# Optimization experiments

Hardware: AMD Instinct MI355X
Metric: run time of the kernel (lower is better)

The kernel has to match this reference:

```python
import jax, jax.numpy as jnp
import numpy as np
import math

B, N, H, D = 2, 2048, 16, 64

def setup_inputs() -> dict:
    key = jax.random.key(0)
    kq, kk, kv = jax.random.split(key, 3)
    q = jax.random.normal(kq, (B, N, H, D), dtype=jnp.float32)
    k = jax.random.normal(kk, (B, N, H, D), dtype=jnp.float32)
    v = jax.random.normal(kv, (B, N, H, D), dtype=jnp.float32)
    return {"q": q, "k": k, "v": v}

def reference(q, k, v):
    d = q.shape[-1]
    # [b,n,h,d] -> [b,h,n,d]
    qh = jnp.transpose(q, (0, 2, 1, 3))
    kh = jnp.transpose(k, (0, 2, 1, 3))
    vh = jnp.transpose(v, (0, 2, 1, 3))
    # scores: [b,h,n,n]
    scores = jnp.einsum('bhqd,bhkd->bhqk', qh, kh) / math.sqrt(d)
    # jax.nn.softmax performs the stable max-subtraction internally,
    # matching the original's explicit max-subtract + softmax.
    attn = jax.nn.softmax(scores, axis=-1)
    o = jnp.einsum('bhqk,bhkd->bhqd', attn, vh)
    # back to [b,n,h,d]
    return jnp.transpose(o, (0, 2, 1, 3))
```

## Files before the change

kernel.cpp:

```cpp
#include <hip/hip_runtime.h>


typedef float  f32x4  __attribute__((ext_vector_type(4)));
typedef float  f32x16 __attribute__((ext_vector_type(16)));
typedef short  s16x8  __attribute__((ext_vector_type(8)));
typedef short  s16x4  __attribute__((ext_vector_type(4)));
typedef int    i32x4  __attribute__((ext_vector_type(4)));

#define QSCALE 0.18033688011112042f

__device__ __forceinline__ unsigned short bf16r(float f) {
    unsigned u = __builtin_bit_cast(unsigned, f);
    u += 0x7fffu + ((u >> 16) & 1u);
    return (unsigned short)(u >> 16);
}

__device__ __forceinline__ s16x8 cvt8f(const float* p) {
    f32x4 a = *(const f32x4*)p;
    f32x4 b = *(const f32x4*)(p + 4);
    s16x8 r;
#pragma unroll
    for (int i = 0; i < 4; ++i) { r[i] = (short)bf16r(a[i]); r[i+4] = (short)bf16r(b[i]); }
    return r;
}

__device__ __forceinline__ s16x8 cvt8f_scaled(const float* p, float s) {
    f32x4 a = *(const f32x4*)p;
    f32x4 b = *(const f32x4*)(p + 4);
    s16x8 r;
#pragma unroll
    for (int i = 0; i < 4; ++i) {
        r[i]   = (short)bf16r(a[i] * s);
        r[i+4] = (short)bf16r(b[i] * s);
    }
    return r;
}

__device__ __forceinline__ void gll16(const unsigned short* g, short* l) {
    __builtin_amdgcn_global_load_lds(
        (const __attribute__((address_space(1))) unsigned int*)g,
        (__attribute__((address_space(3))) unsigned int*)l, 16, 0, 0);
}

__device__ __forceinline__ int pack2(float lo, float hi) {
    unsigned ul = __builtin_bit_cast(unsigned, lo) + 0x8000u;
    unsigned uh = __builtin_bit_cast(unsigned, hi) + 0x8000u;
    return (int)__builtin_amdgcn_perm(uh, ul, 0x07060302u);
}

__global__ void __launch_bounds__(256)
prep(const float* __restrict__ K, const float* __restrict__ V,
     unsigned short* __restrict__ Kt, unsigned short* __restrict__ Vt) {
    const int t = threadIdx.x, bid = blockIdx.x;
    const int bh = bid & 31, nb = bid >> 5;
    const int b = bh >> 4, h = bh & 15;
    const size_t tile0 = ((size_t)bh * 64 + nb * 2) * 2048;

#pragma unroll
    for (int i = 0; i < 2; ++i) {
        const int lin = t * 2 + i;
        const int kbl = lin >> 8, rem = lin & 255;
        const int r = rem >> 3, s = rem & 7;
        const int c = (s - r) & 7;
        const float* src = K + ((size_t)(b * 2048 + nb * 64 + kbl * 32 + r)) * 1024
                             + h * 64 + c * 8;
        *(s16x8*)(Kt + tile0 + kbl * 2048 + r * 64 + s * 8) = cvt8f(src);
    }

    __shared__ short tile[64 * 72];
    {
        const int l16 = t & 15, r = t >> 4;
#pragma unroll
        for (int p = 0; p < 4; ++p) {
            const int key = p * 16 + r;
            const float* vp = V + ((size_t)(b * 2048 + nb * 64 + key)) * 1024
                                + h * 64 + l16 * 4;
            f32x4 x = *(const f32x4*)vp;
#pragma unroll
            for (int i = 0; i < 4; ++i)
                tile[(l16 * 4 + i) * 72 + key] = (short)bf16r(x[i]);
        }
    }
    __syncthreads();
#pragma unroll
    for (int i = 0; i < 4; ++i) {
        const int lin = t * 4 + i;
        const int kbl = lin >> 9, rem = lin & 511;
        const int d = rem >> 3, p = rem & 7;
        const int u = (p - (d >> 1)) & 7;
        s16x4 x = *(const s16x4*)&tile[d * 72 + kbl * 32 + u * 4];
        *(s16x4*)(Vt + tile0 + kbl * 2048 + d * 32 + p * 4) = x;
    }
}

__global__ void __launch_bounds__(256, 2)
attn_fwd(const float* __restrict__ Q, const unsigned short* __restrict__ Kt,
         const unsigned short* __restrict__ Vt, float* __restrict__ O)
{
    __shared__ __align__(16) char smem[65536];

    const int t = threadIdx.x;
    const int w = t >> 6, lane = t & 63;
    const int g = lane >> 5, nl = lane & 31;
    const int qsel = w & 1, ksel = w >> 1;

    const int bid = blockIdx.x;
    const int bh  = bid & 31, qb = bid >> 5;
    const int b   = bh >> 4,  h  = bh & 15;
    const int q0  = qb * 128 + qsel * 64;

    char* wbase = smem + w * 16384;
    short* sKb[2] = { (short*)wbase,            (short*)(wbase + 4096) };
    short* sVb[2] = { (short*)(wbase + 8192),   (short*)(wbase + 12288) };

    s16x8 qf[2][4];
#pragma unroll
    for (int qt = 0; qt < 2; ++qt) {
        const float* qp = Q + ((size_t)(b * 2048 + q0 + qt * 32 + nl)) * 1024
                            + h * 64 + g * 8;
#pragma unroll
        for (int kc = 0; kc < 4; ++kc)
            qf[qt][kc] = cvt8f_scaled(qp + kc * 16, QSCALE);
    }

    int koffr[4];
#pragma unroll
    for (int kc = 0; kc < 4; ++kc)
        koffr[kc] = nl * 64 + ((2 * kc + g + nl) & 7) * 8;
    int voffr[2][2];
#pragma unroll
    for (int s = 0; s < 2; ++s) {
        voffr[s][0] = nl * 32 + (((2 * s + g)     + (nl >> 1)) & 7) * 4;
        voffr[s][1] = nl * 32 + (((4 + 2 * s + g) + (nl >> 1)) & 7) * 4;
    }

    const int lane8 = lane * 8;
    const unsigned short* gbase = Kt + (size_t)bh * 131072;
    const unsigned short* vbase = Vt + (size_t)bh * 131072;

    auto issue = [&](int it, int buf) {
        const int kb = ksel * 32 + it;
        const unsigned short* gk = gbase + (size_t)kb * 2048 + lane8;
        const unsigned short* gv = vbase + (size_t)kb * 2048 + lane8;
#pragma unroll
        for (int i = 0; i < 4; ++i) {
            gll16(gk + i * 512, sKb[buf] + i * 512);
            gll16(gv + i * 512, sVb[buf] + i * 512);
        }
    };

    issue(0, 0);

    f32x16 oa[2][2] = {};
    f32x4 lpv[2] = {};

#pragma unroll 2
    for (int it = 0; it < 32; ++it) {
        const int cur = it & 1;
        const short* bK = sKb[cur];
        const short* bV = sVb[cur];

        asm volatile("s_waitcnt vmcnt(0)" ::: "memory");

        s16x8 kf[4];
#pragma unroll
        for (int kc = 0; kc < 4; ++kc) kf[kc] = *(const s16x8*)&bK[koffr[kc]];
        s16x4 vfl[2][2], vfh[2][2];
#pragma unroll
        for (int dt = 0; dt < 2; ++dt)
#pragma unroll
            for (int s = 0; s < 2; ++s) {
                vfl[dt][s] = *(const s16x4*)&bV[dt * 1024 + voffr[s][0]];
                vfh[dt][s] = *(const s16x4*)&bV[dt * 1024 + voffr[s][1]];
            }

        if (it + 1 < 32) issue(it + 1, cur ^ 1);

        int pk[2][8];
#pragma unroll
        for (int qt = 0; qt < 2; ++qt) {
            f32x16 sacc = {};
#pragma unroll
            for (int kc = 0; kc < 4; ++kc)
                sacc = __builtin_amdgcn_mfma_f32_32x32x16_bf16(kf[kc], qf[qt][kc], sacc, 0, 0, 0);
            float p[16];
#pragma unroll
            for (int r = 0; r < 16; ++r) p[r] = __builtin_amdgcn_exp2f(sacc[r]);
#pragma unroll
            for (int i = 0; i < 4; ++i)
                lpv[qt] += (f32x4){p[4*i], p[4*i+1], p[4*i+2], p[4*i+3]};
#pragma unroll
            for (int i = 0; i < 8; ++i) pk[qt][i] = pack2(p[2*i], p[2*i+1]);
        }

#pragma unroll
        for (int dt = 0; dt < 2; ++dt)
#pragma unroll
            for (int s = 0; s < 2; ++s) {
                s16x8 a = __builtin_shufflevector(vfl[dt][s], vfh[dt][s],
                                                  0, 1, 2, 3, 4, 5, 6, 7);
#pragma unroll
                for (int qt = 0; qt < 2; ++qt) {
                    i32x4 bd = { pk[qt][s*2], pk[qt][s*2+1],
                                 pk[qt][s*2+4], pk[qt][s*2+5] };
                    oa[dt][qt] = __builtin_amdgcn_mfma_f32_32x32x16_bf16(
                        a, __builtin_bit_cast(s16x8, bd), oa[dt][qt], 0, 0, 0);
                }
            }
    }

    float lp[2] = { lpv[0][0] + lpv[0][1] + lpv[0][2] + lpv[0][3],
                    lpv[1][0] + lpv[1][1] + lpv[1][2] + lpv[1][3] };

    __syncthreads();
    float* ex = (float*)smem;
    float* zone = ex + qsel * (64 * 68) + lane * 68;
    if (ksel) {
#pragma unroll
        for (int dt = 0; dt < 2; ++dt)
#pragma unroll
            for (int qt = 0; qt < 2; ++qt)
#pragma unroll
                for (int i = 0; i < 4; ++i)
                    *(f32x4*)(zone + (dt * 2 + qt) * 16 + i * 4) =
                        (f32x4){ oa[dt][qt][4*i],   oa[dt][qt][4*i+1],
                                 oa[dt][qt][4*i+2], oa[dt][qt][4*i+3] };
        zone[64] = lp[0];
        zone[65] = lp[1];
    }
    __syncthreads();
    if (!ksel) {
#pragma unroll
        for (int dt = 0; dt < 2; ++dt)
#pragma unroll
            for (int qt = 0; qt < 2; ++qt)
#pragma unroll
                for (int i = 0; i < 4; ++i) {
                    f32x4 u = *(const f32x4*)(zone + (dt * 2 + qt) * 16 + i * 4);
#pragma unroll
                    for (int j = 0; j < 4; ++j) oa[dt][qt][4*i+j] += u[j];
                }
        float inv[2];
#pragma unroll
        for (int qt = 0; qt < 2; ++qt) {
            float s = lp[qt] + zone[64 + qt];
            s += __shfl_xor(s, 32);
            inv[qt] = 1.0f / s;
        }
#pragma unroll
        for (int qt = 0; qt < 2; ++qt) {
            float* op = O + ((size_t)(b * 2048 + q0 + qt * 32 + nl)) * 1024 + h * 64;
#pragma unroll
            for (int dt = 0; dt < 2; ++dt)
#pragma unroll
                for (int rq = 0; rq < 4; ++rq) {
                    const int d = dt * 32 + 8 * rq + 4 * g;
                    *(f32x4*)(op + d) = (f32x4){
                        oa[dt][qt][4*rq]   * inv[qt], oa[dt][qt][4*rq+1] * inv[qt],
                        oa[dt][qt][4*rq+2] * inv[qt], oa[dt][qt][4*rq+3] * inv[qt] };
                }
        }
    }
}

extern "C" void kernel_launch(void* const* d_in, const int* in_sizes, int n_in,
                              void* d_out, int out_size, void* d_ws, size_t ws_size,
                              hipStream_t stream) {
    const float* q = (const float*)d_in[0];
    const float* k = (const float*)d_in[1];
    const float* v = (const float*)d_in[2];
    float* o = (float*)d_out;

    unsigned short* Kt = (unsigned short*)d_ws;
    unsigned short* Vt = Kt + 4194304;

    hipLaunchKernelGGL(prep,     dim3(1024), dim3(256), 0, stream, k, v, Kt, Vt);
    hipLaunchKernelGGL(attn_fwd, dim3(512),  dim3(256), 0, stream, q, Kt, Vt, o);
}
```

Measured before the change: 134.8 us.

## Load K/V MFMA fragments directly from global, drop LDS staging, halve Q tile

The prep kernel now writes K and V in the exact per-lane MFMA fragment order, so the attention kernel reads fragments straight from global memory into registers with a two-stage software pipeline. This replaces the per-wave global_load_lds double buffering and its waitcnt stalls. Each wave now handles 32 queries instead of 64, the grid doubles to 1024 blocks, LDS shrinks to a small reduction buffer, and launch bounds rise to 3 blocks per CU. Softmax packing uses the hardware v_cvt_pk_bf16_f32 instruction. The trade-off is that each K/V fragment is reused across only one Q tile, which doubles K/V traffic that L2 must absorb, and global load latency is now exposed in registers rather than hidden by LDS.

```diff
diff --git a/kernel.cpp b/kernel.cpp
--- a/kernel.cpp
+++ b/kernel.cpp
@@ -36,16 +36,10 @@
     return r;
 }
 
-__device__ __forceinline__ void gll16(const unsigned short* g, short* l) {
-    __builtin_amdgcn_global_load_lds(
-        (const __attribute__((address_space(1))) unsigned int*)g,
-        (__attribute__((address_space(3))) unsigned int*)l, 16, 0, 0);
-}
-
-__device__ __forceinline__ int pack2(float lo, float hi) {
-    unsigned ul = __builtin_bit_cast(unsigned, lo) + 0x8000u;
-    unsigned uh = __builtin_bit_cast(unsigned, hi) + 0x8000u;
-    return (int)__builtin_amdgcn_perm(uh, ul, 0x07060302u);
+__device__ __forceinline__ int cvtpk2(float lo, float hi) {
+    int r;
+    asm("v_cvt_pk_bf16_f32 %0, %1, %2" : "=v"(r) : "v"(lo), "v"(hi));
+    return r;
 }
 
 __global__ void __launch_bounds__(256)
@@ -60,11 +54,11 @@
     for (int i = 0; i < 2; ++i) {
         const int lin = t * 2 + i;
         const int kbl = lin >> 8, rem = lin & 255;
-        const int r = rem >> 3, s = rem & 7;
-        const int c = (s - r) & 7;
-        const float* src = K + ((size_t)(b * 2048 + nb * 64 + kbl * 32 + r)) * 1024
-                             + h * 64 + c * 8;
-        *(s16x8*)(Kt + tile0 + kbl * 2048 + r * 64 + s * 8) = cvt8f(src);
+        const int kc = rem >> 6, l = rem & 63;
+        const int nl = l & 31, gg = l >> 5;
+        const float* src = K + ((size_t)(b * 2048 + nb * 64 + kbl * 32 + nl)) * 1024
+                             + h * 64 + kc * 16 + gg * 8;
+        *(s16x8*)(Kt + tile0 + kbl * 2048 + kc * 512 + l * 8) = cvt8f(src);
     }
 
     __shared__ short tile[64 * 72];
@@ -77,27 +71,31 @@
                                 + h * 64 + l16 * 4;
             f32x4 x = *(const f32x4*)vp;
 #pragma unroll
-            for (int i = 0; i < 4; ++i)
-                tile[(l16 * 4 + i) * 72 + key] = (short)bf16r(x[i]);
+            for (int i2 = 0; i2 < 4; ++i2)
+                tile[(l16 * 4 + i2) * 72 + key] = (short)bf16r(x[i2]);
         }
     }
     __syncthreads();
 #pragma unroll
-    for (int i = 0; i < 4; ++i) {
-        const int lin = t * 4 + i;
-        const int kbl = lin >> 9, rem = lin & 511;
-        const int d = rem >> 3, p = rem & 7;
-        const int u = (p - (d >> 1)) & 7;
-        s16x4 x = *(const s16x4*)&tile[d * 72 + kbl * 32 + u * 4];
-        *(s16x4*)(Vt + tile0 + kbl * 2048 + d * 32 + p * 4) = x;
-    }
-}
-
-__global__ void __launch_bounds__(256, 2)
+    for (int i = 0; i < 2; ++i) {
+        const int lin = t * 2 + i;
+        const int kbl = lin >> 8, rem = lin & 255;
+        const int qq = rem >> 6, l = rem & 63;
+        const int dt = qq >> 1, s = qq & 1;
+        const int nl = l & 31, gg = l >> 5;
+        const int base = (dt * 32 + nl) * 72 + kbl * 32 + 8 * s + 4 * gg;
+        s16x4 lo = *(const s16x4*)&tile[base];
+        s16x4 hi = *(const s16x4*)&tile[base + 16];
+        *(s16x8*)(Vt + tile0 + kbl * 2048 + qq * 512 + l * 8) =
+            __builtin_shufflevector(lo, hi, 0, 1, 2, 3, 4, 5, 6, 7);
+    }
+}
+
+__global__ void __launch_bounds__(256, 3)
 attn_fwd(const float* __restrict__ Q, const unsigned short* __restrict__ Kt,
          const unsigned short* __restrict__ Vt, float* __restrict__ O)
 {
-    __shared__ __align__(16) char smem[65536];
+    __shared__ __align__(16) float ex[2 * 64 * 36];
 
     const int t = threadIdx.x;
     const int w = t >> 6, lane = t & 63;
@@ -107,158 +105,98 @@
     const int bid = blockIdx.x;
     const int bh  = bid & 31, qb = bid >> 5;
     const int b   = bh >> 4,  h  = bh & 15;
-    const int q0  = qb * 128 + qsel * 64;
-
-    char* wbase = smem + w * 16384;
-    short* sKb[2] = { (short*)wbase,            (short*)(wbase + 4096) };
-    short* sVb[2] = { (short*)(wbase + 8192),   (short*)(wbase + 12288) };
-
-    s16x8 qf[2][4];
-#pragma unroll
-    for (int qt = 0; qt < 2; ++qt) {
-        const float* qp = Q + ((size_t)(b * 2048 + q0 + qt * 32 + nl)) * 1024
-                            + h * 64 + g * 8;
+    const int q0  = qb * 64 + qsel * 32;
+
+    s16x8 qf[4];
+    {
+        const float* qp = Q + ((size_t)(b * 2048 + q0 + nl)) * 1024 + h * 64 + g * 8;
 #pragma unroll
         for (int kc = 0; kc < 4; ++kc)
-            qf[qt][kc] = cvt8f_scaled(qp + kc * 16, QSCALE);
-    }
-
-    int koffr[4];
-#pragma unroll
-    for (int kc = 0; kc < 4; ++kc)
-        koffr[kc] = nl * 64 + ((2 * kc + g + nl) & 7) * 8;
-    int voffr[2][2];
-#pragma unroll
-    for (int s = 0; s < 2; ++s) {
-        voffr[s][0] = nl * 32 + (((2 * s + g)     + (nl >> 1)) & 7) * 4;
-        voffr[s][1] = nl * 32 + (((4 + 2 * s + g) + (nl >> 1)) & 7) * 4;
-    }
-
-    const int lane8 = lane * 8;
-    const unsigned short* gbase = Kt + (size_t)bh * 131072;
-    const unsigned short* vbase = Vt + (size_t)bh * 131072;
-
-    auto issue = [&](int it, int buf) {
-        const int kb = ksel * 32 + it;
-        const unsigned short* gk = gbase + (size_t)kb * 2048 + lane8;
-        const unsigned short* gv = vbase + (size_t)kb * 2048 + lane8;
+            qf[kc] = cvt8f_scaled(qp + kc * 16, QSCALE);
+    }
+
+    const unsigned short* kp = Kt + (size_t)bh * 131072 + (size_t)ksel * 65536 + lane * 8;
+    const unsigned short* vp = Vt + (size_t)bh * 131072 + (size_t)ksel * 65536 + lane * 8;
+
+    f32x16 oa0 = {}, oa1 = {};
+    float lp = 0.f;
+
+    s16x8 kfa[4], vfa[4], kfb[4], vfb[4];
+
+#define LOADT(KD, VD, IT) do {                                              \
+        const unsigned short* _k = kp + (IT) * 2048;                        \
+        const unsigned short* _v = vp + (IT) * 2048;                        \
+        _Pragma("unroll")                                                   \
+        for (int _i = 0; _i < 4; ++_i) {                                    \
+            KD[_i] = *(const s16x8*)(_k + _i * 512);                        \
+            VD[_i] = *(const s16x8*)(_v + _i * 512);                        \
+        } } while (0)
+
+#define STEP(KF, VF) do {                                                   \
+        f32x16 sacc = {};                                                   \
+        _Pragma("unroll")                                                   \
+        for (int _kc = 0; _kc < 4; ++_kc)                                   \
+            sacc = __builtin_amdgcn_mfma_f32_32x32x16_bf16(                 \
+                KF[_kc], qf[_kc], sacc, 0, 0, 0);                           \
+        float pr[16];                                                       \
+        _Pragma("unroll")                                                   \
+        for (int _r = 0; _r < 16; ++_r) pr[_r] = __builtin_amdgcn_exp2f(sacc[_r]); \
+        _Pragma("unroll")                                                   \
+        for (int _r = 0; _r < 16; ++_r) lp += pr[_r];                       \
+        int pk[8];                                                          \
+        _Pragma("unroll")                                                   \
+        for (int _i = 0; _i < 8; ++_i) pk[_i] = cvtpk2(pr[2*_i], pr[2*_i+1]); \
+        _Pragma("unroll")                                                   \
+        for (int _s = 0; _s < 2; ++_s) {                                    \
+            i32x4 bd = { pk[_s*2], pk[_s*2+1], pk[_s*2+4], pk[_s*2+5] };    \
+            s16x8 bb = __builtin_bit_cast(s16x8, bd);                       \
+            oa0 = __builtin_amdgcn_mfma_f32_32x32x16_bf16(VF[_s],     bb, oa0, 0, 0, 0); \
+            oa1 = __builtin_amdgcn_mfma_f32_32x32x16_bf16(VF[2 + _s], bb, oa1, 0, 0, 0); \
+        } } while (0)
+
+    LOADT(kfa, vfa, 0);
+    for (int it = 0; it < 32; it += 2) {
+        LOADT(kfb, vfb, it + 1);
+        STEP(kfa, vfa);
+        if (it + 2 < 32) LOADT(kfa, vfa, it + 2);
+        STEP(kfb, vfb);
+    }
+#undef LOADT
+#undef STEP
+
+    float* zone = ex + qsel * (64 * 36) + lane * 36;
+    if (ksel) {
 #pragma unroll
         for (int i = 0; i < 4; ++i) {
-            gll16(gk + i * 512, sKb[buf] + i * 512);
-            gll16(gv + i * 512, sVb[buf] + i * 512);
-        }
-    };
-
-    issue(0, 0);
-
-    f32x16 oa[2][2] = {};
-    f32x4 lpv[2] = {};
-
-#pragma unroll 2
-    for (int it = 0; it < 32; ++it) {
-        const int cur = it & 1;
-        const short* bK = sKb[cur];
-        const short* bV = sVb[cur];
-
-        asm volatile("s_waitcnt vmcnt(0)" ::: "memory");
-
-        s16x8 kf[4];
-#pragma unroll
-        for (int kc = 0; kc < 4; ++kc) kf[kc] = *(const s16x8*)&bK[koffr[kc]];
-        s16x4 vfl[2][2], vfh[2][2];
-#pragma unroll
-        for (int dt = 0; dt < 2; ++dt)
-#pragma unroll
-            for (int s = 0; s < 2; ++s) {
-                vfl[dt][s] = *(const s16x4*)&bV[dt * 1024 + voffr[s][0]];
-                vfh[dt][s] = *(const s16x4*)&bV[dt * 1024 + voffr[s][1]];
-            }
-
-        if (it + 1 < 32) issue(it + 1, cur ^ 1);
-
-        int pk[2][8];
-#pragma unroll
-        for (int qt = 0; qt < 2; ++qt) {
-            f32x16 sacc = {};
-#pragma unroll
-            for (int kc = 0; kc < 4; ++kc)
-                sacc = __builtin_amdgcn_mfma_f32_32x32x16_bf16(kf[kc], qf[qt][kc], sacc, 0, 0, 0);
-            float p[16];
-#pragma unroll
-            for (int r = 0; r < 16; ++r) p[r] = __builtin_amdgcn_exp2f(sacc[r]);
-#pragma unroll
-            for (int i = 0; i < 4; ++i)
-                lpv[qt] += (f32x4){p[4*i], p[4*i+1], p[4*i+2], p[4*i+3]};
-#pragma unroll
-            for (int i = 0; i < 8; ++i) pk[qt][i] = pack2(p[2*i], p[2*i+1]);
-        }
-
-#pragma unroll
-        for (int dt = 0; dt < 2; ++dt)
-#pragma unroll
-            for (int s = 0; s < 2; ++s) {
-                s16x8 a = __builtin_shufflevector(vfl[dt][s], vfh[dt][s],
-                                                  0, 1, 2, 3, 4, 5, 6, 7);
-#pragma unroll
-                for (int qt = 0; qt < 2; ++qt) {
-                    i32x4 bd = { pk[qt][s*2], pk[qt][s*2+1],
-                                 pk[qt][s*2+4], pk[qt][s*2+5] };
-                    oa[dt][qt] = __builtin_amdgcn_mfma_f32_32x32x16_bf16(
-                        a, __builtin_bit_cast(s16x8, bd), oa[dt][qt], 0, 0, 0);
-                }
-            }
-    }
-
-    float lp[2] = { lpv[0][0] + lpv[0][1] + lpv[0][2] + lpv[0][3],
-                    lpv[1][0] + lpv[1][1] + lpv[1][2] + lpv[1][3] };
-
-    __syncthreads();
-    float* ex = (float*)smem;
-    float* zone = ex + qsel * (64 * 68) + lane * 68;
-    if (ksel) {
-#pragma unroll
-        for (int dt = 0; dt < 2; ++dt)
-#pragma unroll
-            for (int qt = 0; qt < 2; ++qt)
-#pragma unroll
-                for (int i = 0; i < 4; ++i)
-                    *(f32x4*)(zone + (dt * 2 + qt) * 16 + i * 4) =
-                        (f32x4){ oa[dt][qt][4*i],   oa[dt][qt][4*i+1],
-                                 oa[dt][qt][4*i+2], oa[dt][qt][4*i+3] };
-        zone[64] = lp[0];
-        zone[65] = lp[1];
+            *(f32x4*)(zone + i * 4) =
+                (f32x4){ oa0[4*i], oa0[4*i+1], oa0[4*i+2], oa0[4*i+3] };
+            *(f32x4*)(zone + 16 + i * 4) =
+                (f32x4){ oa1[4*i], oa1[4*i+1], oa1[4*i+2], oa1[4*i+3] };
+        }
+        zone[32] = lp;
     }
     __syncthreads();
     if (!ksel) {
 #pragma unroll
-        for (int dt = 0; dt < 2; ++dt)
-#pragma unroll
-            for (int qt = 0; qt < 2; ++qt)
-#pragma unroll
-                for (int i = 0; i < 4; ++i) {
-                    f32x4 u = *(const f32x4*)(zone + (dt * 2 + qt) * 16 + i * 4);
-#pragma unroll
-                    for (int j = 0; j < 4; ++j) oa[dt][qt][4*i+j] += u[j];
-                }
-        float inv[2];
-#pragma unroll
-        for (int qt = 0; qt < 2; ++qt) {
-            float s = lp[qt] + zone[64 + qt];
-            s += __shfl_xor(s, 32);
-            inv[qt] = 1.0f / s;
-        }
-#pragma unroll
-        for (int qt = 0; qt < 2; ++qt) {
-            float* op = O + ((size_t)(b * 2048 + q0 + qt * 32 + nl)) * 1024 + h * 64;
-#pragma unroll
-            for (int dt = 0; dt < 2; ++dt)
-#pragma unroll
-                for (int rq = 0; rq < 4; ++rq) {
-                    const int d = dt * 32 + 8 * rq + 4 * g;
-                    *(f32x4*)(op + d) = (f32x4){
-                        oa[dt][qt][4*rq]   * inv[qt], oa[dt][qt][4*rq+1] * inv[qt],
-                        oa[dt][qt][4*rq+2] * inv[qt], oa[dt][qt][4*rq+3] * inv[qt] };
-                }
+        for (int i = 0; i < 4; ++i) {
+            f32x4 u0 = *(const f32x4*)(zone + i * 4);
+            f32x4 u1 = *(const f32x4*)(zone + 16 + i * 4);
+#pragma unroll
+            for (int j = 0; j < 4; ++j) { oa0[4*i+j] += u0[j]; oa1[4*i+j] += u1[j]; }
+        }
+        float ssum = lp + zone[32];
+        ssum += __shfl_xor(ssum, 32);
+        const float inv = 1.0f / ssum;
+        float* op = O + ((size_t)(b * 2048 + q0 + nl)) * 1024 + h * 64;
+#pragma unroll
+        for (int rq = 0; rq < 4; ++rq) {
+            const int d0 = 8 * rq + 4 * g;
+            *(f32x4*)(op + d0) = (f32x4){
+                oa0[4*rq]   * inv, oa0[4*rq+1] * inv,
+                oa0[4*rq+2] * inv, oa0[4*rq+3] * inv };
+            *(f32x4*)(op + 32 + d0) = (f32x4){
+                oa1[4*rq]   * inv, oa1[4*rq+1] * inv,
+                oa1[4*rq+2] * inv, oa1[4*rq+3] * inv };
         }
     }
 }
@@ -275,5 +213,5 @@
     unsigned short* Vt = Kt + 4194304;
 
     hipLaunchKernelGGL(prep,     dim3(1024), dim3(256), 0, stream, k, v, Kt, Vt);
-    hipLaunchKernelGGL(attn_fwd, dim3(512),  dim3(256), 0, stream, q, Kt, Vt, o);
-}
+    hipLaunchKernelGGL(attn_fwd, dim3(1024), dim3(256), 0, stream, q, Kt, Vt, o);
+}
```

Result: no change. 137.0 us (+1.6%).
